# Kernel tuning notes

Hardware: AMD Instinct MI355X
Metric: run time of the kernel (lower is better)

Reference implementation:

```python
import jax, jax.numpy as jnp
from jax import lax
import numpy as np

EPS = 1e-6

def _sym(A):
    return 0.5 * (A + jnp.swapaxes(A, -1, -2))

def _eigh_apply(A, fn):
    # apply fn to eigenvalues of a symmetric PD matrix batch
    w, v = jnp.linalg.eigh(_sym(A))
    w = jnp.maximum(w, EPS)
    return jnp.einsum('...ij,...j,...kj->...ik', v, fn(w), v)

def _sqrt_invsqrt(A):
    w, v = jnp.linalg.eigh(_sym(A))
    w = jnp.maximum(w, EPS)
    s = jnp.sqrt(w)
    As = jnp.einsum('...ij,...j,...kj->...ik', v, s, v)
    Ais = jnp.einsum('...ij,...j,...kj->...ik', v, 1.0 / s, v)
    return As, Ais

def _geodesic(A, B, t):
    # SPD geodesic from A toward B at parameter t: A^1/2 (A^-1/2 B A^-1/2)^t A^1/2
    # t broadcastable against eigenvalue axis [..., n]
    As, Ais = _sqrt_invsqrt(A)
    C = _sym(Ais @ B @ Ais)
    w, v = jnp.linalg.eigh(C)
    w = jnp.maximum(w, EPS)
    Ct = jnp.einsum('...ij,...j,...kj->...ik', v, w ** t, v)
    return _sym(As @ Ct @ As)

def weight_normalize(W):
    # vectorized equivalent of the per-row clamp loop in the torch source
    return jnp.clip(W, 0.001, 0.999)

def recursive_fm(x, W):
    # recursive Frechet mean: M_1 = X_1, M_k = geodesic(M_{k-1}, X_k, w_k / sum_{i<=k} w_i)
    # x: [B, I, n, n] SPD, W: [O, I] positive weights -> [B, O, n, n]
    B, I, n, _ = x.shape
    O = W.shape[0]
    t = W / jnp.cumsum(W, axis=1)  # [O, I], t[:, 0] == 1
    M0 = jnp.broadcast_to(x[:, 0, None], (B, O, n, n))
    xs = (jnp.moveaxis(x[:, 1:], 1, 0), jnp.swapaxes(t[:, 1:], 0, 1))  # [I-1,B,n,n], [I-1,O]

    def step(M, inp):
        xk, tk = inp  # [B, n, n], [O]
        Xb = jnp.broadcast_to(xk[:, None], M.shape)
        return _geodesic(M, Xb, tk[None, :, None]), None

    M, _ = lax.scan(step, M0, xs)
    return M

def fast_fm(x, W):
    # fast (log-Euclidean) weighted Frechet mean: expm(sum_i w_i logm(X_i) / sum_i w_i)
    L = _eigh_apply(x, jnp.log)  # [B, I, n, n]
    Wn = W / jnp.sum(W, axis=1, keepdims=True)
    M = jnp.einsum('oi,bimn->bomn', Wn, L)  # [B, O, n, n]
    w, v = jnp.linalg.eigh(_sym(M))
    return jnp.einsum('...ij,...j,...kj->...ik', v, jnp.exp(w), v)

def spd_linear_forward(x, weight_matrix):
    Wn = weight_normalize(weight_matrix)
    out3 = fast_fm(x, Wn)
    out1 = recursive_fm(x, Wn)
    out2 = recursive_fm(jnp.flip(x, 1), jnp.flip(Wn, 1))
    return (out1, out2, out3)

def setup_inputs():
    key = jax.random.key(0)
    k1, k2 = jax.random.split(key)
    B, I, O, n = 256, 32, 32, 32
    A = jax.random.normal(k1, (B, I, n, n), dtype=jnp.float32)
    # well-conditioned SPD inputs: A A^T / n + 0.5 I
    x = jnp.einsum('bimk,bink->bimn', A, A) / n + 0.5 * jnp.eye(n, dtype=jnp.float32)
    weight_matrix = jax.random.uniform(k2, (O, I), dtype=jnp.float32)  # torch.rand init
    return {"x": x, "weight_matrix": weight_matrix}

def reference(x, weight_matrix):
    return spd_linear_forward(x, weight_matrix)
```

## Files before the change

### kernel.cpp

```cpp
#include <hip/hip_runtime.h>
#include <math.h>

#define NN 32
#define PADL 36
#define PADT 33
#define NSWEEP 6

__device__ __forceinline__ void jacobi_sweeps(float g[NN], float &nrm) {
  const int lane = threadIdx.x;
  {
    float a0=0.f,a1=0.f,a2=0.f,a3=0.f;
    #pragma unroll
    for (int i = 0; i < NN; i += 4) {
      a0 = fmaf(g[i+0],g[i+0],a0); a1 = fmaf(g[i+1],g[i+1],a1);
      a2 = fmaf(g[i+2],g[i+2],a2); a3 = fmaf(g[i+3],g[i+3],a3);
    }
    nrm = (a0+a1)+(a2+a3);
  }
  #pragma unroll 1
  for (int sw = 0; sw < NSWEEP; ++sw) {
    #pragma unroll 1
    for (int m = 1; m < NN; ++m) {
      float p[NN];
      #pragma unroll
      for (int i = 0; i < NN; ++i) p[i] = __shfl_xor(g[i], m);
      float d0=0.f,d1=0.f,d2=0.f,d3=0.f;
      #pragma unroll
      for (int i = 0; i < NN; i += 4) {
        d0 = fmaf(g[i+0], p[i+0], d0); d1 = fmaf(g[i+1], p[i+1], d1);
        d2 = fmaf(g[i+2], p[i+2], d2); d3 = fmaf(g[i+3], p[i+3], d3);
      }
      float d = (d0+d1)+(d2+d3);
      float other = __shfl_xor(nrm, m);
      bool isP = (((lane ^ m) & 31) > (lane & 31));
      float pn = isP ? nrm : other;
      float qn = isP ? other : nrm;
      float delta = pn - qn;
      float R   = sqrtf(fmaf(delta, delta, 4.f*d*d));
      float den = delta + copysignf(R + 1e-30f, delta);
      float t = -2.f*d / den;
      float c = rsqrtf(fmaf(t, t, 1.f));
      float s = t * c;
      float sg = isP ? -s : s;
      #pragma unroll
      for (int i = 0; i < NN; ++i) g[i] = fmaf(sg, p[i], c*g[i]);
      float csd2 = 2.f*c*s*d;
      nrm = c*c*nrm + s*s*other + (isP ? -csd2 : csd2);
    }
  }
  float a0=0.f,a1=0.f,a2=0.f,a3=0.f;
  #pragma unroll
  for (int i = 0; i < NN; i += 4) {
    a0 = fmaf(g[i+0],g[i+0],a0); a1 = fmaf(g[i+1],g[i+1],a1);
    a2 = fmaf(g[i+2],g[i+2],a2); a3 = fmaf(g[i+3],g[i+3],a3);
  }
  nrm = (a0+a1)+(a2+a3);
}

__device__ __forceinline__ void cholesky32(float m[NN], float *Lbuf, int l5) {
  #pragma unroll
  for (int j = 0; j < NN; ++j) {
    float bj   = __shfl(m[j], j, 32);
    float invd = rsqrtf(bj);
    float lkj  = m[j] * invd;
    bool isj = (l5 == j), gt = (l5 > j);
    #pragma unroll
    for (int i = j; i < NN; ++i) {
      float bi  = __shfl(m[i], j, 32);
      float lij = bi * invd;
      float upd = fmaf(-lij, lkj, m[i]);
      m[i] = isj ? lij : (gt ? upd : m[i]);
    }
    if (isj) Lbuf[j*PADL + 32] = invd;
  }
  #pragma unroll
  for (int i = 0; i < NN; i += 4)
    *(float4*)&Lbuf[l5*PADL + i] = make_float4(m[i], m[i+1], m[i+2], m[i+3]);
}

__device__ __forceinline__ void trsv32(float x[NN], const float *Lbuf) {
  #pragma unroll
  for (int j = 0; j < NN; ++j) {
    float yj = x[j] * Lbuf[j*PADL + 32];
    x[j] = yj;
    #pragma unroll
    for (int i0 = ((j+1) & ~3); i0 < NN; i0 += 4) {
      float4 Lc = *(const float4*)&Lbuf[j*PADL + i0];
      if (i0+0 > j) x[i0+0] = fmaf(-Lc.x, yj, x[i0+0]);
      if (i0+1 > j) x[i0+1] = fmaf(-Lc.y, yj, x[i0+1]);
      if (i0+2 > j) x[i0+2] = fmaf(-Lc.z, yj, x[i0+2]);
      if (i0+3 > j) x[i0+3] = fmaf(-Lc.w, yj, x[i0+3]);
    }
  }
}

__device__ __forceinline__ void transpose32(float x[NN], float *Tbuf, int l5) {
  __syncthreads();
  #pragma unroll
  for (int i = 0; i < NN; ++i) Tbuf[l5*PADT + i] = x[i];
  __syncthreads();
  #pragma unroll
  for (int i = 0; i < NN; ++i) x[i] = Tbuf[i*PADT + l5];
}

__device__ __forceinline__ void trmul_L(const float us[NN], float z[NN], const float *Lbuf) {
  #pragma unroll
  for (int i = 0; i < NN; ++i) z[i] = 0.f;
  #pragma unroll
  for (int k = 0; k < NN; ++k) {
    float uk = us[k];
    #pragma unroll
    for (int i0 = (k & ~3); i0 < NN; i0 += 4) {
      float4 Lc = *(const float4*)&Lbuf[k*PADL + i0];
      if (i0+0 >= k) z[i0+0] = fmaf(Lc.x, uk, z[i0+0]);
      if (i0+1 >= k) z[i0+1] = fmaf(Lc.y, uk, z[i0+1]);
      if (i0+2 >= k) z[i0+2] = fmaf(Lc.z, uk, z[i0+2]);
      if (i0+3 >= k) z[i0+3] = fmaf(Lc.w, uk, z[i0+3]);
    }
  }
}

__device__ __forceinline__ void zzT(const float z[NN], float out[NN], float *Tbuf, int l5) {
  __syncthreads();
  #pragma unroll
  for (int i = 0; i < NN; ++i) Tbuf[l5*PADT + i] = z[i];
  __syncthreads();
  #pragma unroll
  for (int i = 0; i < NN; ++i) out[i] = 0.f;
  #pragma unroll 1
  for (int k = 0; k < NN; ++k) {
    float zjk = Tbuf[k*PADT + l5];
    #pragma unroll
    for (int i = 0; i < NN; ++i)
      out[i] = fmaf(Tbuf[k*PADT + i], zjk, out[i]);
  }
}

__global__ void k_tables(const float* __restrict__ W, float* __restrict__ tfwd,
                         float* __restrict__ trev, float* __restrict__ wnn) {
  int o = threadIdx.x;
  if (o >= NN) return;
  float w[NN];
  #pragma unroll 1
  for (int i = 0; i < NN; ++i) w[i] = fminf(fmaxf(W[o*NN+i], 0.001f), 0.999f);
  float cs = 0.f;
  #pragma unroll 1
  for (int i = 0; i < NN; ++i) { cs += w[i]; tfwd[o*NN+i] = w[i]/cs; }
  float tot = cs;
  #pragma unroll 1
  for (int i = 0; i < NN; ++i) wnn[o*NN+i] = w[i]/tot;
  cs = 0.f;
  #pragma unroll 1
  for (int i = 0; i < NN; ++i) { cs += w[NN-1-i]; trev[o*NN+i] = w[NN-1-i]/cs; }
}

__global__ __launch_bounds__(64) void k_logm(const float* __restrict__ x,
                                             float* __restrict__ llog) {
  __shared__ float Tbuf[2][NN*PADT];
  int lane = threadIdx.x, half = lane >> 5, l5 = lane & 31;
  int P = blockIdx.x*2 + half;
  const float* xp = x + (size_t)P*1024 + l5;
  float g[NN];
  #pragma unroll
  for (int i = 0; i < NN; ++i) g[i] = xp[i*NN];
  float nrm;
  jacobi_sweeps(g, nrm);
  float lg   = 0.5f * log2f(fmaxf(nrm, 1e-12f));
  float lnl  = lg * 0.69314718056f;
  float invl = exp2f(-lg);
  float *Tb = Tbuf[half];
  __syncthreads();
  #pragma unroll
  for (int i = 0; i < NN; ++i) Tb[l5*PADT + i] = g[i]*invl;
  Tb[l5*PADT + 32] = lnl;
  __syncthreads();
  float m[NN];
  #pragma unroll
  for (int i = 0; i < NN; ++i) m[i] = 0.f;
  #pragma unroll 1
  for (int k = 0; k < NN; ++k) {
    float coef = Tb[k*PADT + 32] * Tb[k*PADT + l5];
    #pragma unroll
    for (int i = 0; i < NN; ++i) m[i] = fmaf(Tb[k*PADT + i], coef, m[i]);
  }
  float* op = llog + (size_t)P*1024 + l5;
  #pragma unroll
  for (int i = 0; i < NN; ++i) op[i*NN] = m[i];
}

__global__ __launch_bounds__(64) void k_fastfm(const float* __restrict__ llog,
                                               const float* __restrict__ wnn,
                                               float* __restrict__ out3) {
  __shared__ float Tbuf[2][NN*PADT];
  int lane = threadIdx.x, half = lane >> 5, l5 = lane & 31;
  int P = blockIdx.x*2 + half;
  int b = P >> 5, o = P & 31;
  float acc[NN];
  #pragma unroll
  for (int i = 0; i < NN; ++i) acc[i] = 0.f;
  const float* lp = llog + (size_t)b*NN*1024 + l5;
  #pragma unroll 1
  for (int i2 = 0; i2 < NN; ++i2) {
    float w = wnn[o*NN + i2];
    const float* q = lp + (size_t)i2*1024;
    #pragma unroll
    for (int i = 0; i < NN; ++i) acc[i] = fmaf(q[i*NN], w, acc[i]);
  }
  #pragma unroll
  for (int i = 0; i < NN; ++i) acc[i] += (i == l5) ? 4.0f : 0.0f;
  float nrm;
  jacobi_sweeps(acc, nrm);
  float lg  = 0.5f * log2f(fmaxf(nrm, 1e-12f));
  float lam = exp2f(lg);
  float sc  = expf(0.5f*(lam - 4.0f)) * exp2f(-lg);
  #pragma unroll
  for (int i = 0; i < NN; ++i) acc[i] *= sc;
  float m3[NN];
  zzT(acc, m3, Tbuf[half], l5);
  float* op = out3 + (size_t)P*1024 + l5;
  #pragma unroll
  for (int i = 0; i < NN; ++i) op[i*NN] = m3[i];
}

__global__ __launch_bounds__(64) void k_recursive(const float* __restrict__ x,
    const float* __restrict__ tfwd, const float* __restrict__ trev,
    float* __restrict__ out1, float* __restrict__ out2) {
  __shared__ float Lbuf[2][NN*PADL];
  __shared__ float Tbuf[2][NN*PADT];
  int lane = threadIdx.x, half = lane >> 5, l5 = lane & 31;
  int P = blockIdx.x*2 + half;
  int dir = P >> 13;
  int rem = P & 8191;
  int b = rem >> 5, o = rem & 31;
  const float* tt = dir ? trev : tfwd;
  float* outp = (dir ? out2 : out1) + (size_t)(b*NN + o)*1024;
  const float* xb = x + (size_t)b*NN*1024;
  float *Lb = Lbuf[half], *Tb = Tbuf[half];

  float m[NN];
  {
    const float* xp = xb + (size_t)(dir ? (NN-1) : 0)*1024 + l5;
    #pragma unroll
    for (int i = 0; i < NN; ++i) m[i] = xp[i*NN];
  }
  #pragma unroll 1
  for (int j = 1; j < NN; ++j) {
    int k = dir ? (NN-1-j) : j;
    float xk[NN];
    const float* xp = xb + (size_t)k*1024 + l5;
    #pragma unroll
    for (int i = 0; i < NN; ++i) xk[i] = xp[i*NN];
    float tv = tt[o*NN + j];

    cholesky32(m, Lb, l5);

    #pragma unroll 1
    for (int pass = 0; pass < 2; ++pass) {
      trsv32(xk, Lb);
      if (pass == 0) transpose32(xk, Tb, l5);
    }

    float nrm;
    jacobi_sweeps(xk, nrm);
    float lg = 0.5f * log2f(fmaxf(nrm, 1e-12f));
    float sc = exp2f(lg * (0.5f*tv - 1.0f));
    #pragma unroll
    for (int i = 0; i < NN; ++i) xk[i] *= sc;

    float z[NN];
    trmul_L(xk, z, Lb);
    zzT(z, m, Tb, l5);
  }
  #pragma unroll
  for (int i = 0; i < NN; ++i) outp[i*NN + l5] = m[i];
}

extern "C" void kernel_launch(void* const* d_in, const int* in_sizes, int n_in,
                              void* d_out, int out_size, void* d_ws, size_t ws_size,
                              hipStream_t stream) {
  (void)in_sizes; (void)n_in; (void)out_size; (void)ws_size;
  const float* x = (const float*)d_in[0];
  const float* W = (const float*)d_in[1];
  float* out  = (float*)d_out;
  float* ws   = (float*)d_ws;
  float* tfwd = ws;
  float* trev = ws + 1024;
  float* wnn  = ws + 2048;
  float* out1 = out;
  float* out2 = out + 8388608;
  float* out3 = out + 16777216;
  float* llog = out1;

  hipLaunchKernelGGL(k_tables,    dim3(1),    dim3(64), 0, stream, W, tfwd, trev, wnn);
  hipLaunchKernelGGL(k_logm,      dim3(4096), dim3(64), 0, stream, x, llog);
  hipLaunchKernelGGL(k_fastfm,    dim3(4096), dim3(64), 0, stream, llog, wnn, out3);
  hipLaunchKernelGGL(k_recursive, dim3(8192), dim3(64), 0, stream, x, tfwd, trev, out1, out2);
}
```

Measured before the change: 30.41 ms.

## Precompute input Cholesky factors and use single-sided whitening in recursive geodesic

Adds a kernel that Cholesky-factors every input matrix once. The recursive kernel then whitens the factor R_k with a single triangular solve, so Jacobi runs on L^-1 R rather than the full congruence L^-1 X L^-T, which removes a transpose and a second solve per step. The Jacobi sweeps switch to ds_bpermute, use fast reciprocal and rsqrt, and exit early when no rotation is significant. Shared-memory transposes use float2 stores with a new padding. This needs a large workspace buffer and keeps a fallback path; the early exit and approximate math may change accuracy slightly.

```diff
diff --git a/kernel.cpp b/kernel.cpp
--- a/kernel.cpp
+++ b/kernel.cpp
@@ -3,11 +3,15 @@
 
 #define NN 32
 #define PADL 36
-#define PADT 33
+#define PADT 34
 #define NSWEEP 6
 
+__device__ __forceinline__ float bperm(int addr, float x) {
+  return __int_as_float(__builtin_amdgcn_ds_bpermute(addr, __float_as_int(x)));
+}
+
 __device__ __forceinline__ void jacobi_sweeps(float g[NN], float &nrm) {
-  const int lane = threadIdx.x;
+  const int lane = threadIdx.x & 63;
   {
     float a0=0.f,a1=0.f,a2=0.f,a3=0.f;
     #pragma unroll
@@ -19,11 +23,13 @@
   }
   #pragma unroll 1
   for (int sw = 0; sw < NSWEEP; ++sw) {
+    bool act = false;
     #pragma unroll 1
     for (int m = 1; m < NN; ++m) {
+      const int addr = ((lane ^ m) << 2);
       float p[NN];
       #pragma unroll
-      for (int i = 0; i < NN; ++i) p[i] = __shfl_xor(g[i], m);
+      for (int i = 0; i < NN; ++i) p[i] = bperm(addr, g[i]);
       float d0=0.f,d1=0.f,d2=0.f,d3=0.f;
       #pragma unroll
       for (int i = 0; i < NN; i += 4) {
@@ -31,14 +37,17 @@
         d2 = fmaf(g[i+2], p[i+2], d2); d3 = fmaf(g[i+3], p[i+3], d3);
       }
       float d = (d0+d1)+(d2+d3);
-      float other = __shfl_xor(nrm, m);
-      bool isP = (((lane ^ m) & 31) > (lane & 31));
+      float other = bperm(addr, nrm);
+      const bool isP = (((lane ^ m) & 31) > (lane & 31));
       float pn = isP ? nrm : other;
       float qn = isP ? other : nrm;
       float delta = pn - qn;
-      float R   = sqrtf(fmaf(delta, delta, 4.f*d*d));
+      float dd = d * d;
+      act = act || (dd > 1e-10f * (pn * qn));
+      float r2 = fmaf(delta, delta, 4.f * dd);
+      float R  = r2 * rsqrtf(fmaxf(r2, 1e-37f));
       float den = delta + copysignf(R + 1e-30f, delta);
-      float t = -2.f*d / den;
+      float t = (-2.f * d) * __builtin_amdgcn_rcpf(den);
       float c = rsqrtf(fmaf(t, t, 1.f));
       float s = t * c;
       float sg = isP ? -s : s;
@@ -47,6 +56,7 @@
       float csd2 = 2.f*c*s*d;
       nrm = c*c*nrm + s*s*other + (isP ? -csd2 : csd2);
     }
+    if (!__any(act)) break;
   }
   float a0=0.f,a1=0.f,a2=0.f,a3=0.f;
   #pragma unroll
@@ -58,12 +68,14 @@
 }
 
 __device__ __forceinline__ void cholesky32(float m[NN], float *Lbuf, int l5) {
+  float myinvd = 0.f;
   #pragma unroll
   for (int j = 0; j < NN; ++j) {
     float bj   = __shfl(m[j], j, 32);
     float invd = rsqrtf(bj);
     float lkj  = m[j] * invd;
     bool isj = (l5 == j), gt = (l5 > j);
+    myinvd = isj ? invd : myinvd;
     #pragma unroll
     for (int i = j; i < NN; ++i) {
       float bi  = __shfl(m[i], j, 32);
@@ -71,11 +83,11 @@
       float upd = fmaf(-lij, lkj, m[i]);
       m[i] = isj ? lij : (gt ? upd : m[i]);
     }
-    if (isj) Lbuf[j*PADL + 32] = invd;
   }
   #pragma unroll
   for (int i = 0; i < NN; i += 4)
     *(float4*)&Lbuf[l5*PADL + i] = make_float4(m[i], m[i+1], m[i+2], m[i+3]);
+  Lbuf[l5*PADL + 32] = myinvd;
 }
 
 __device__ __forceinline__ void trsv32(float x[NN], const float *Lbuf) {
@@ -97,7 +109,8 @@
 __device__ __forceinline__ void transpose32(float x[NN], float *Tbuf, int l5) {
   __syncthreads();
   #pragma unroll
-  for (int i = 0; i < NN; ++i) Tbuf[l5*PADT + i] = x[i];
+  for (int i = 0; i < NN; i += 2)
+    *(float2*)&Tbuf[l5*PADT + i] = make_float2(x[i], x[i+1]);
   __syncthreads();
   #pragma unroll
   for (int i = 0; i < NN; ++i) x[i] = Tbuf[i*PADT + l5];
@@ -123,7 +136,8 @@
 __device__ __forceinline__ void zzT(const float z[NN], float out[NN], float *Tbuf, int l5) {
   __syncthreads();
   #pragma unroll
-  for (int i = 0; i < NN; ++i) Tbuf[l5*PADT + i] = z[i];
+  for (int i = 0; i < NN; i += 2)
+    *(float2*)&Tbuf[l5*PADT + i] = make_float2(z[i], z[i+1]);
   __syncthreads();
   #pragma unroll
   for (int i = 0; i < NN; ++i) out[i] = 0.f;
@@ -131,8 +145,11 @@
   for (int k = 0; k < NN; ++k) {
     float zjk = Tbuf[k*PADT + l5];
     #pragma unroll
-    for (int i = 0; i < NN; ++i)
-      out[i] = fmaf(Tbuf[k*PADT + i], zjk, out[i]);
+    for (int i = 0; i < NN; i += 2) {
+      float2 c2 = *(const float2*)&Tbuf[k*PADT + i];
+      out[i+0] = fmaf(c2.x, zjk, out[i+0]);
+      out[i+1] = fmaf(c2.y, zjk, out[i+1]);
+    }
   }
 }
 
@@ -171,7 +188,8 @@
   float *Tb = Tbuf[half];
   __syncthreads();
   #pragma unroll
-  for (int i = 0; i < NN; ++i) Tb[l5*PADT + i] = g[i]*invl;
+  for (int i = 0; i < NN; i += 2)
+    *(float2*)&Tb[l5*PADT + i] = make_float2(g[i]*invl, g[i+1]*invl);
   Tb[l5*PADT + 32] = lnl;
   __syncthreads();
   float m[NN];
@@ -181,7 +199,11 @@
   for (int k = 0; k < NN; ++k) {
     float coef = Tb[k*PADT + 32] * Tb[k*PADT + l5];
     #pragma unroll
-    for (int i = 0; i < NN; ++i) m[i] = fmaf(Tb[k*PADT + i], coef, m[i]);
+    for (int i = 0; i < NN; i += 2) {
+      float2 c2 = *(const float2*)&Tb[k*PADT + i];
+      m[i+0] = fmaf(c2.x, coef, m[i+0]);
+      m[i+1] = fmaf(c2.y, coef, m[i+1]);
+    }
   }
   float* op = llog + (size_t)P*1024 + l5;
   #pragma unroll
@@ -222,10 +244,82 @@
   for (int i = 0; i < NN; ++i) op[i*NN] = m3[i];
 }
 
-__global__ __launch_bounds__(64) void k_recursive(const float* __restrict__ x,
+__global__ __launch_bounds__(64) void k_cholx(const float* __restrict__ x,
+                                              float* __restrict__ Rg) {
+  int lane = threadIdx.x, half = lane >> 5, l5 = lane & 31;
+  int P = blockIdx.x*2 + half;
+  const float* xp = x + (size_t)P*1024 + l5;
+  float m[NN];
+  #pragma unroll
+  for (int i = 0; i < NN; ++i) m[i] = xp[i*NN];
+  #pragma unroll
+  for (int j = 0; j < NN; ++j) {
+    float bj   = __shfl(m[j], j, 32);
+    float invd = rsqrtf(bj);
+    float lkj  = m[j] * invd;
+    bool isj = (l5 == j), gt = (l5 > j);
+    #pragma unroll
+    for (int i = j; i < NN; ++i) {
+      float bi  = __shfl(m[i], j, 32);
+      float lij = bi * invd;
+      float upd = fmaf(-lij, lkj, m[i]);
+      m[i] = isj ? lij : (gt ? upd : m[i]);
+    }
+  }
+  float* op = Rg + (size_t)P*1024 + l5;
+  #pragma unroll
+  for (int i = 0; i < NN; ++i) op[i*NN] = (i >= l5) ? m[i] : 0.f;
+}
+
+__global__ __launch_bounds__(64) void k_rec_pre(const float* __restrict__ Rg,
     const float* __restrict__ tfwd, const float* __restrict__ trev,
     float* __restrict__ out1, float* __restrict__ out2) {
-  __shared__ float Lbuf[2][NN*PADL];
+  __shared__ __align__(16) float Ub[2][NN*PADL];
+  int lane = threadIdx.x, half = lane >> 5, l5 = lane & 31;
+  int P = blockIdx.x*2 + half;
+  int dir = P >> 13;
+  int rem = P & 8191;
+  int b = rem >> 5, o = rem & 31;
+  const float* tt = dir ? trev : tfwd;
+  float* outp = (dir ? out2 : out1) + (size_t)(b*NN + o)*1024;
+  const float* Rb = Rg + (size_t)b*NN*1024;
+  float *Uh = Ub[half];
+
+  float m[NN], rk[NN];
+  {
+    const float* rp = Rb + (size_t)(dir ? (NN-1) : 0)*1024 + l5;
+    #pragma unroll
+    for (int i = 0; i < NN; ++i) rk[i] = rp[i*NN];
+    zzT(rk, m, Uh, l5);
+  }
+  #pragma unroll 1
+  for (int j = 1; j < NN; ++j) {
+    int k = dir ? (NN-1-j) : j;
+    const float* rp = Rb + (size_t)k*1024 + l5;
+    #pragma unroll
+    for (int i = 0; i < NN; ++i) rk[i] = rp[i*NN];
+    float tv = tt[o*NN + j];
+
+    cholesky32(m, Uh, l5);
+    trsv32(rk, Uh);
+    float nrm;
+    jacobi_sweeps(rk, nrm);
+    float lg = log2f(fmaxf(nrm, 1e-12f));
+    float sc = exp2f(lg * 0.5f * (tv - 1.0f));
+    #pragma unroll
+    for (int i = 0; i < NN; ++i) rk[i] *= sc;
+    float z[NN];
+    trmul_L(rk, z, Uh);
+    zzT(z, m, Uh, l5);
+  }
+  #pragma unroll
+  for (int i = 0; i < NN; ++i) outp[i*NN + l5] = m[i];
+}
+
+__global__ __launch_bounds__(64) void k_rec_fb(const float* __restrict__ x,
+    const float* __restrict__ tfwd, const float* __restrict__ trev,
+    float* __restrict__ out1, float* __restrict__ out2) {
+  __shared__ __align__(16) float Lbuf[2][NN*PADL];
   __shared__ float Tbuf[2][NN*PADT];
   int lane = threadIdx.x, half = lane >> 5, l5 = lane & 31;
   int P = blockIdx.x*2 + half;
@@ -253,20 +347,15 @@
     float tv = tt[o*NN + j];
 
     cholesky32(m, Lb, l5);
-
-    #pragma unroll 1
-    for (int pass = 0; pass < 2; ++pass) {
-      trsv32(xk, Lb);
-      if (pass == 0) transpose32(xk, Tb, l5);
-    }
-
+    trsv32(xk, Lb);
+    transpose32(xk, Tb, l5);
+    trsv32(xk, Lb);
     float nrm;
     jacobi_sweeps(xk, nrm);
     float lg = 0.5f * log2f(fmaxf(nrm, 1e-12f));
     float sc = exp2f(lg * (0.5f*tv - 1.0f));
     #pragma unroll
     for (int i = 0; i < NN; ++i) xk[i] *= sc;
-
     float z[NN];
     trmul_L(xk, z, Lb);
     zzT(z, m, Tb, l5);
@@ -278,7 +367,7 @@
 extern "C" void kernel_launch(void* const* d_in, const int* in_sizes, int n_in,
                               void* d_out, int out_size, void* d_ws, size_t ws_size,
                               hipStream_t stream) {
-  (void)in_sizes; (void)n_in; (void)out_size; (void)ws_size;
+  (void)in_sizes; (void)n_in; (void)out_size;
   const float* x = (const float*)d_in[0];
   const float* W = (const float*)d_in[1];
   float* out  = (float*)d_out;
@@ -286,13 +375,22 @@
   float* tfwd = ws;
   float* trev = ws + 1024;
   float* wnn  = ws + 2048;
+  float* Rg   = ws + 3072;
   float* out1 = out;
   float* out2 = out + 8388608;
   float* out3 = out + 16777216;
   float* llog = out1;
 
+  const size_t need = (size_t)(3072 + 8388608) * sizeof(float);
+  const bool pre = (ws_size >= need);
+
   hipLaunchKernelGGL(k_tables,    dim3(1),    dim3(64), 0, stream, W, tfwd, trev, wnn);
   hipLaunchKernelGGL(k_logm,      dim3(4096), dim3(64), 0, stream, x, llog);
   hipLaunchKernelGGL(k_fastfm,    dim3(4096), dim3(64), 0, stream, llog, wnn, out3);
-  hipLaunchKernelGGL(k_recursive, dim3(8192), dim3(64), 0, stream, x, tfwd, trev, out1, out2);
-}
+  if (pre) {
+    hipLaunchKernelGGL(k_cholx,   dim3(4096), dim3(64), 0, stream, x, Rg);
+    hipLaunchKernelGGL(k_rec_pre, dim3(8192), dim3(64), 0, stream, Rg, tfwd, trev, out1, out2);
+  } else {
+    hipLaunchKernelGGL(k_rec_fb,  dim3(8192), dim3(64), 0, stream, x, tfwd, trev, out1, out2);
+  }
+}
```

Result: slower. 32.35 ms (+6.4%).
